# Kernel optimization log

Hardware: AMD Instinct MI355X
Metric: run time of the kernel (lower is better)

The kernel has to match this reference:

```python
import jax, jax.numpy as jnp
import numpy as np

N = 4096        # atoms
F = 128         # node feature channels (MACE hidden irreps scalar channels)
K = 8           # radial basis size
NELEM = 10      # chemical elements
RMAX = 5.0      # cutoff (Angstrom), model.r_max
BOX = 34.5      # box side -> ~0.1 atoms/A^3, ~50 neighbors within RMAX


def setup_inputs() -> dict:
    key = jax.random.key(0)
    ks = jax.random.split(key, 7)
    positions = jax.random.uniform(ks[0], (N, 3), jnp.float32) * BOX
    z = jax.random.randint(ks[1], (N,), 0, NELEM)
    embed = jax.random.normal(ks[2], (NELEM, F), jnp.float32) * 0.1
    W1 = jax.random.normal(ks[3], (K, F, F), jnp.float32) / np.sqrt(K * F)
    W2 = jax.random.normal(ks[4], (K, F, F), jnp.float32) / np.sqrt(K * F)
    Wr1 = jax.random.normal(ks[5], (F, F), jnp.float32) / np.sqrt(F)
    Wr2 = jax.random.normal(ks[6], (F, 1), jnp.float32) / np.sqrt(F)
    return dict(positions=positions, z=z, embed=embed, W1=W1, W2=W2, Wr1=Wr1, Wr2=Wr2)


def _energy(positions, embed, W1, W2, Wr1, Wr2, z):
    # node embedding from atomic species (node_attrs one-hot @ embedding)
    h = embed[z]                                            # [N,F]
    # --- neighborlist: radius graph with self-edge masking (pbc = False) ---
    sq = jnp.sum(positions * positions, axis=-1)            # [N]
    d2 = sq[:, None] + sq[None, :] - 2.0 * (positions @ positions.T)  # [N,N]
    eye = jnp.eye(positions.shape[0], dtype=bool)
    d2_safe = jnp.where(eye | (d2 <= 0), 1.0, d2)           # avoid sqrt(0) grad
    d = jnp.sqrt(d2_safe)                                   # [N,N]
    mask = (d < RMAX) & (~eye) & (d2 > 0)                   # keep_edge = ~true_self_edge
    # smooth cutoff envelope
    env = jnp.where(mask, 0.5 * (jnp.cos(jnp.pi * d / RMAX) + 1.0), 0.0)  # [N,N]
    # Gaussian radial basis
    mus = jnp.linspace(0.0, RMAX, K, dtype=jnp.float32)     # [K]
    gamma = jnp.float32((K / RMAX) ** 2)
    rbf = jnp.exp(-gamma * (d[..., None] - mus) ** 2) * env[..., None]    # [N,N,K]
    # --- two message-passing layers (radial-weighted neighbor aggregation) ---
    for W in (W1, W2):
        A = jnp.einsum('ijk,jf->ikf', rbf, h)               # [N,K,F] gather-scatter agg
        h = jax.nn.silu(jnp.einsum('ikf,kfg->ig', A, W) + h)  # [N,F]
    # --- per-atom energy readout, summed over graph ---
    e_atom = (jax.nn.silu(h @ Wr1) @ Wr2)[:, 0]             # [N]
    return jnp.sum(e_atom)


def reference(positions, z, embed, W1, W2, Wr1, Wr2):
    energy, dE_dpos = jax.value_and_grad(_energy)(positions, embed, W1, W2, Wr1, Wr2, z)
    forces = -dE_dpos                                       # [N,3]
    return energy, forces
```

## Files before the change

### kernel.cpp

```cpp
#include <hip/hip_runtime.h>
#include <math.h>

#define N_ATOMS 4096
#define F 128
#define K 8
#define KF 1024
#define KFF 131072
#define FF 16384
#define NF 524288
#define NKF 4194304
#define MAXNB 128
#define RMAX 5.0f
#define RMAX2 25.0f
#define GAMMA 2.56f
#define MU_STEP 0.714285714285714f
#define PI_F 3.14159265358979323846f
#define POR (PI_F / RMAX)

typedef __bf16 bf16x8_t __attribute__((ext_vector_type(8)));
typedef float f32x4_t __attribute__((ext_vector_type(4)));
typedef unsigned short u16x8_t __attribute__((ext_vector_type(8)));
typedef unsigned short u16x4_t __attribute__((ext_vector_type(4)));

__device__ __forceinline__ float sigm(float x){ return 1.0f/(1.0f + expf(-x)); }
__device__ __forceinline__ unsigned short f2bf(float x){
  unsigned int u = __float_as_uint(x);
  u += 0x7fff + ((u >> 16) & 1);
  return (unsigned short)(u >> 16);
}


__device__ __forceinline__ void agg_body(int a, int t,
        const float* __restrict__ h_in, const int* __restrict__ nb_idx,
        const float* __restrict__ rbf, const int* __restrict__ nb_cnt,
        unsigned short* __restrict__ Af){
  int grp = t >> 6, lane = t & 63;
  __shared__ int s_j[MAXNB];
  __shared__ float s_acc[4][8][128];
  int cnt = nb_cnt[a];
  for (int idx = t; idx < cnt; idx += 256) s_j[idx] = nb_idx[a*MAXNB + idx];
  __syncthreads();
  float2 acc[8];
  #pragma unroll
  for (int k = 0; k < 8; k++) acc[k] = {0.f, 0.f};
  const float4* rb = (const float4*)(rbf + (size_t)a*MAXNB*8);
  for (int n = grp; n < cnt; n += 4){
    float2 hv = *(const float2*)&h_in[(size_t)s_j[n]*F + lane*2];
    float4 r0 = rb[n*2], r1 = rb[n*2+1];
    acc[0].x += r0.x*hv.x; acc[0].y += r0.x*hv.y;
    acc[1].x += r0.y*hv.x; acc[1].y += r0.y*hv.y;
    acc[2].x += r0.z*hv.x; acc[2].y += r0.z*hv.y;
    acc[3].x += r0.w*hv.x; acc[3].y += r0.w*hv.y;
    acc[4].x += r1.x*hv.x; acc[4].y += r1.x*hv.y;
    acc[5].x += r1.y*hv.x; acc[5].y += r1.y*hv.y;
    acc[6].x += r1.z*hv.x; acc[6].y += r1.z*hv.y;
    acc[7].x += r1.w*hv.x; acc[7].y += r1.w*hv.y;
  }
  #pragma unroll
  for (int k = 0; k < 8; k++)
    *(float2*)&s_acc[grp][k][lane*2] = acc[k];
  __syncthreads();
  int k = t >> 5, q = t & 31;
  int f0 = q*4;
  float v[4];
  #pragma unroll
  for (int i = 0; i < 4; i++){
    int f = f0 + i;
    v[i] = s_acc[0][k][f] + s_acc[1][k][f] + s_acc[2][k][f] + s_acc[3][k][f];
  }
  int lf = (a & 15) | (((f0 >> 3) & 3) << 4);
  int kc = k*4 + (f0 >> 5);
  size_t flat = (size_t)(a >> 4)*16384 + ((size_t)kc*64 + lf)*8 + (f0 & 7);
  u16x4_t o;
  o[0] = f2bf(v[0]); o[1] = f2bf(v[1]); o[2] = f2bf(v[2]); o[3] = f2bf(v[3]);
  *(u16x4_t*)(Af + flat) = o;
}

__device__ __forceinline__ void mgemm_bwd_body(int bx, int t,
        const unsigned short* __restrict__ Gf, const unsigned short* __restrict__ Bf,
        unsigned short* __restrict__ dAbf){
  int l = t & 63, w = t >> 6;
  int rtile = (bx & 63)*4 + w;
  int nt0 = (bx >> 6)*8;
  f32x4_t acc[8];
  #pragma unroll
  for (int i = 0; i < 8; i++) acc[i] = (f32x4_t){0.f,0.f,0.f,0.f};
  const unsigned short* Ab = Gf + (size_t)rtile*2048 + l*8;
  const unsigned short* Bb = Bf + l*8;
  #pragma unroll
  for (int kc = 0; kc < 4; kc++){
    bf16x8_t a = *(const bf16x8_t*)(Ab + kc*512);
    #pragma unroll
    for (int nt = 0; nt < 8; nt++){
      bf16x8_t b = *(const bf16x8_t*)(Bb + (kc*64 + nt0 + nt)*512);
      acc[nt] = __builtin_amdgcn_mfma_f32_16x16x32_bf16(a, b, acc[nt], 0, 0, 0);
    }
  }
  int row0 = rtile*16 + (l >> 4)*4;
  int col = l & 15;
  #pragma unroll
  for (int nt = 0; nt < 8; nt++){
    #pragma unroll
    for (int r = 0; r < 4; r++)
      dAbf[(size_t)(row0+r)*1024 + (nt0+nt)*16 + col] = f2bf(acc[nt][r]);
  }
}


__global__ __launch_bounds__(256) void k_prep(const float* __restrict__ pos,
        const int* __restrict__ z, const float* __restrict__ embed,
        const float* __restrict__ W1, const float* __restrict__ W2,
        const float* __restrict__ Wr1,
        int* __restrict__ nb_idx, float* __restrict__ nb_d, int* __restrict__ nb_cnt,
        float* __restrict__ rbf, float* __restrict__ drbf,
        unsigned short* __restrict__ WF1, unsigned short* __restrict__ WF2,
        unsigned short* __restrict__ WDF2, unsigned short* __restrict__ WTF1,
        unsigned short* __restrict__ WTF2, unsigned short* __restrict__ Wr1F,
        unsigned short* __restrict__ Wr1TF,
        float* __restrict__ h0, unsigned short* __restrict__ h0bf){
  int t = threadIdx.x;
  if (blockIdx.x < 1024){
    int w = t >> 6, lane = t & 63;
    int i = blockIdx.x*4 + w;
    __shared__ float spx[256], spy[256], spz[256], ssq[256];
    float pix = pos[3*i], piy = pos[3*i+1], piz = pos[3*i+2];
    float sqi = pix*pix + piy*piy + piz*piz;
    int count = 0;
    for (int jb = 0; jb < N_ATOMS; jb += 256){
      __syncthreads();
      float px = pos[3*(jb+t)], py = pos[3*(jb+t)+1], pz = pos[3*(jb+t)+2];
      spx[t] = px; spy[t] = py; spz[t] = pz;
      ssq[t] = px*px + py*py + pz*pz;
      __syncthreads();
      #pragma unroll
      for (int c = 0; c < 4; c++){
        int jj = c*64 + lane;
        int j = jb + jj;
        float dot = pix*spx[jj] + piy*spy[jj] + piz*spz[jj];
        float d2 = sqi + ssq[jj] - 2.0f*dot;
        bool pred = (j != i) && (d2 > 0.0f) && (d2 < RMAX2);
        unsigned long long m = __ballot(pred);
        int off = __popcll(m & ((1ull << lane) - 1ull));
        if (pred){
          int p = count + off;
          if (p < MAXNB){ nb_idx[i*MAXNB + p] = j; nb_d[i*MAXNB + p] = sqrtf(d2); }
        }
        count += __popcll(m);
      }
    }
    int cc = count > MAXNB ? MAXNB : count;
    if (lane == 0) nb_cnt[i] = cc;
    __syncthreads();
    for (int n = lane; n < cc; n += 64){
      float d = nb_d[i*MAXNB + n];
      float ph = POR*d;
      float cph, sph;
      __sincosf(ph, &sph, &cph);
      float env = 0.5f*(cph + 1.0f);
      float denv = -0.5f*POR*sph;
      float rr[8], dd[8];
      #pragma unroll
      for (int k = 0; k < 8; k++){
        float dm = d - MU_STEP*(float)k;
        float G = expf(-GAMMA*dm*dm);
        rr[k] = G*env;
        dd[k] = G*(-2.0f*GAMMA*dm*env + denv);
      }
      float4* rb = (float4*)(rbf + ((size_t)i*MAXNB + n)*8);
      rb[0] = {rr[0],rr[1],rr[2],rr[3]};
      rb[1] = {rr[4],rr[5],rr[6],rr[7]};
      float4* db = (float4*)(drbf + ((size_t)i*MAXNB + n)*8);
      db[0] = {dd[0],dd[1],dd[2],dd[3]};
      db[1] = {dd[4],dd[5],dd[6],dd[7]};
    }
    return;
  }
  if (blockIdx.x >= 1088){
    int idx = (blockIdx.x - 1088)*256 + t;
    int i = idx >> 7, f = idx & 127;
    float v = embed[z[i]*F + f];
    h0[idx] = v;
    h0bf[idx] = f2bf(v);
    return;
  }
  int idx = (blockIdx.x - 1024)*256 + t;
  int l = idx & 63;
  int hi = idx >> 6;
  {
    int kc = hi >> 3, nt = hi & 7;
    int kfb = kc*32 + ((l>>4)&3)*8;
    int g = nt*16 + (l&15);
    u16x8_t v1, v2, vd;
    #pragma unroll
    for (int j = 0; j < 8; j++){
      int kf = kfb + j;
      v1[j] = f2bf(W1[kf*128 + g]);
      v2[j] = f2bf(W2[kf*128 + g]);
      vd[j] = f2bf(W2[(kf>>7)*FF + g*F + (kf&127)]);
    }
    *(u16x8_t*)(WF1 + idx*8) = v1;
    *(u16x8_t*)(WF2 + idx*8) = v2;
    *(u16x8_t*)(WDF2 + idx*8) = vd;
  }
  {
    int kc = hi >> 6, nt = hi & 63;
    int gb = kc*32 + ((l>>4)&3)*8;
    int kf = nt*16 + (l&15);
    u16x8_t t1, t2;
    #pragma unroll
    for (int j = 0; j < 8; j++){
      int g = gb + j;
      t1[j] = f2bf(W1[kf*128 + g]);
      t2[j] = f2bf(W2[kf*128 + g]);
    }
    *(u16x8_t*)(WTF1 + idx*8) = t1;
    *(u16x8_t*)(WTF2 + idx*8) = t2;
  }
  {
    int m = idx >> 9;
    int ll = (idx >> 3) & 63;
    int j = idx & 7;
    int kc = m >> 3, nt = m & 7;
    int kf = kc*32 + ((ll>>4)&3)*8 + j;
    int g = nt*16 + (ll&15);
    Wr1F[idx]  = f2bf(Wr1[kf*128 + g]);
    Wr1TF[idx] = f2bf(Wr1[g*128 + kf]);
  }
}

__global__ __launch_bounds__(256) void k_agg(const float* __restrict__ h_in,
        const int* __restrict__ nb_idx, const float* __restrict__ rbf,
        const int* __restrict__ nb_cnt, unsigned short* __restrict__ Af){
  agg_body(blockIdx.x, threadIdx.x, h_in, nb_idx, rbf, nb_cnt, Af);
}

__global__ __launch_bounds__(256) void k_bwdmix(const unsigned short* __restrict__ Gf,
        const unsigned short* __restrict__ Bf, unsigned short* __restrict__ dAbf,
        const float* __restrict__ g2b, const int* __restrict__ nb_idx,
        const float* __restrict__ rbf, const int* __restrict__ nb_cnt,
        unsigned short* __restrict__ Af){
  if (blockIdx.x < 512){
    mgemm_bwd_body(blockIdx.x, threadIdx.x, Gf, Bf, dAbf);
    return;
  }
  agg_body(blockIdx.x - 512, threadIdx.x, g2b, nb_idx, rbf, nb_cnt, Af);
}

__global__ __launch_bounds__(256) void k_mgemm_bwd(const unsigned short* __restrict__ Gf,
        const unsigned short* __restrict__ Bf, unsigned short* __restrict__ dAbf){
  mgemm_bwd_body(blockIdx.x, threadIdx.x, Gf, Bf, dAbf);
}

__global__ __launch_bounds__(256) void k_mgemm_fwd(const unsigned short* __restrict__ Af,
        const unsigned short* __restrict__ Bf, const float* __restrict__ addv,
        const float* __restrict__ msrc, float* __restrict__ out_m,
        float* __restrict__ out_h, unsigned short* __restrict__ out_hbf,
        unsigned short* __restrict__ out_frag, int mode){
  int t = threadIdx.x;
  int l = t & 63, w = t >> 6;
  int rtile = blockIdx.x;
  int nt = blockIdx.y*4 + w;
  f32x4_t accA = (f32x4_t){0.f,0.f,0.f,0.f};
  f32x4_t accB = (f32x4_t){0.f,0.f,0.f,0.f};
  const unsigned short* Ab = Af + (size_t)rtile*16384 + l*8;
  const unsigned short* Bb = Bf + l*8;
  #pragma unroll
  for (int kc = 0; kc < 32; kc += 2){
    bf16x8_t a0 = *(const bf16x8_t*)(Ab + kc*512);
    bf16x8_t b0 = *(const bf16x8_t*)(Bb + (kc*8 + nt)*512);
    bf16x8_t a1 = *(const bf16x8_t*)(Ab + (kc+1)*512);
    bf16x8_t b1 = *(const bf16x8_t*)(Bb + ((kc+1)*8 + nt)*512);
    accA = __builtin_amdgcn_mfma_f32_16x16x32_bf16(a0, b0, accA, 0, 0, 0);
    accB = __builtin_amdgcn_mfma_f32_16x16x32_bf16(a1, b1, accB, 0, 0, 0);
  }
  f32x4_t acc = accA + accB;
  int row0 = rtile*16 + (l >> 4)*4;
  int col = nt*16 + (l & 15);
  if (mode == 0){
    #pragma unroll
    for (int r = 0; r < 4; r++){
      int i = row0 + r;
      float m = acc[r] + addv[(size_t)i*F + col];
      out_m[(size_t)i*F + col] = m;
      float h = m*sigm(m);
      out_h[(size_t)i*F + col] = h;
      out_hbf[(size_t)i*F + col] = f2bf(h);
    }
  } else {
    int kc2 = col >> 5;
    int lfr0 = (((col >> 3) & 3) << 4);
    int jj = col & 7;
    #pragma unroll
    for (int r = 0; r < 4; r++){
      int i = row0 + r;
      float mm = msrc[(size_t)i*F + col];
      float sg = sigm(mm);
      float gv = (acc[r] + addv[(size_t)i*F + col])*(sg*(1.f + mm*(1.f - sg)));
      int lfr = (i & 15) | lfr0;
      size_t flat = (((size_t)(i>>4)*4 + kc2)*64 + lfr)*8 + jj;
      out_frag[flat] = f2bf(gv);
    }
  }
}

__global__ __launch_bounds__(64) void k_readout(const unsigned short* __restrict__ h2bf,
        const float* __restrict__ m2, const unsigned short* __restrict__ Wr1F,
        const unsigned short* __restrict__ Wr1TF, const float* __restrict__ Wr2,
        float* __restrict__ e_at, float* __restrict__ g2,
        unsigned short* __restrict__ g2frag){
  int a0 = blockIdx.x*16;
  int l = threadIdx.x;
  int rl = l & 15;
  __shared__ unsigned short sdu[16][136];
  f32x4_t acc[8];
  #pragma unroll
  for (int nt = 0; nt < 8; nt++) acc[nt] = (f32x4_t){0.f,0.f,0.f,0.f};
  #pragma unroll
  for (int kc = 0; kc < 4; kc++){
    bf16x8_t af = *(const bf16x8_t*)(h2bf + (size_t)(a0+rl)*F + kc*32 + ((l>>4)&3)*8);
    #pragma unroll
    for (int nt = 0; nt < 8; nt++){
      bf16x8_t bf = *(const bf16x8_t*)(Wr1F + ((kc*8+nt)*64 + l)*8);
      acc[nt] = __builtin_amdgcn_mfma_f32_16x16x32_bf16(af, bf, acc[nt], 0, 0, 0);
    }
  }
  float epart[4] = {0.f,0.f,0.f,0.f};
  #pragma unroll
  for (int nt = 0; nt < 8; nt++){
    float w2 = Wr2[nt*16 + rl];
    #pragma unroll
    for (int r = 0; r < 4; r++){
      float u = acc[nt][r];
      float sg = sigm(u);
      epart[r] += u*sg*w2;
      sdu[(l>>4)*4 + r][nt*16 + rl] = f2bf(w2*(sg*(1.f + u*(1.f - sg))));
    }
  }
  #pragma unroll
  for (int o = 1; o < 16; o <<= 1){
    #pragma unroll
    for (int r = 0; r < 4; r++) epart[r] += __shfl_xor(epart[r], o);
  }
  if (rl == 0){
    #pragma unroll
    for (int r = 0; r < 4; r++) e_at[a0 + (l>>4)*4 + r] = epart[r];
  }
  __syncthreads();
  f32x4_t acc2[8];
  #pragma unroll
  for (int nt = 0; nt < 8; nt++) acc2[nt] = (f32x4_t){0.f,0.f,0.f,0.f};
  #pragma unroll
  for (int kc = 0; kc < 4; kc++){
    bf16x8_t af = *(const bf16x8_t*)&sdu[rl][kc*32 + ((l>>4)&3)*8];
    #pragma unroll
    for (int nt = 0; nt < 8; nt++){
      bf16x8_t bf = *(const bf16x8_t*)(Wr1TF + ((kc*8+nt)*64 + l)*8);
      acc2[nt] = __builtin_amdgcn_mfma_f32_16x16x32_bf16(af, bf, acc2[nt], 0, 0, 0);
    }
  }
  #pragma unroll
  for (int nt = 0; nt < 8; nt++){
    int g = nt*16 + rl;
    int kc2 = g >> 5;
    int lfr0 = (((g >> 3) & 3) << 4);
    int jj = g & 7;
    #pragma unroll
    for (int r = 0; r < 4; r++){
      int a = a0 + (l>>4)*4 + r;
      float mm = m2[(size_t)a*F + g];
      float sg = sigm(mm);
      float gv = acc2[nt][r]*(sg*(1.f + mm*(1.f - sg)));
      g2[(size_t)a*F + g] = gv;
      int lfr = (a & 15) | lfr0;
      g2frag[(((size_t)(a>>4)*4 + kc2)*64 + lfr)*8 + jj] = f2bf(gv);
    }
  }
}

__global__ __launch_bounds__(256) void k_edge(const unsigned short* __restrict__ dA2bf,
        const unsigned short* __restrict__ dA1bf, const unsigned short* __restrict__ h1bf,
        const unsigned short* __restrict__ h0bf, const float* __restrict__ drbf,
        const int* __restrict__ nb_idx, const int* __restrict__ nb_cnt,
        float* __restrict__ edge_s){
  int a = blockIdx.x;
  int t = threadIdx.x;
  int w = t >> 6, l = t & 63;
  __shared__ int s_j[MAXNB];
  int cnt = nb_cnt[a];
  for (int idx = t; idx < cnt; idx += 256) s_j[idx] = nb_idx[a*MAXNB + idx];
  int r = l & 15;
  int sel = (l >> 4) & 3;
  u16x8_t a2u[4], a1u[4];
  #pragma unroll
  for (int kc = 0; kc < 4; kc++){
    u16x8_t v2 = {0,0,0,0,0,0,0,0};
    u16x8_t v1 = {0,0,0,0,0,0,0,0};
    if (r < 8){
      v2 = *(const u16x8_t*)(dA2bf + (size_t)a*KF + r*F + kc*32 + sel*8);
      v1 = *(const u16x8_t*)(dA1bf + (size_t)a*KF + r*F + kc*32 + sel*8);
    }
    a2u[kc] = v2; a1u[kc] = v1;
  }
  __syncthreads();
  for (int n0 = w*16; n0 < cnt; n0 += 64){
    int nl = n0 + r;
    int nls = nl < cnt ? nl : cnt - 1;
    int j = s_j[nls];
    const unsigned short* h1p = h1bf + (size_t)j*F + sel*8;
    const unsigned short* h0p = h0bf + (size_t)j*F + sel*8;
    f32x4_t acc = (f32x4_t){0.f,0.f,0.f,0.f};
    #pragma unroll
    for (int kc = 0; kc < 4; kc++){
      bf16x8_t b = *(const bf16x8_t*)(h1p + kc*32);
      acc = __builtin_amdgcn_mfma_f32_16x16x32_bf16(*(const bf16x8_t*)&a2u[kc], b, acc, 0, 0, 0);
    }
    #pragma unroll
    for (int kc = 0; kc < 4; kc++){
      bf16x8_t b = *(const bf16x8_t*)(h0p + kc*32);
      acc = __builtin_amdgcn_mfma_f32_16x16x32_bf16(*(const bf16x8_t*)&a1u[kc], b, acc, 0, 0, 0);
    }
    int krow = (l >> 4) * 4;
    float part = 0.f;
    if (krow < 8){
      float4 dr = *(const float4*)(drbf + ((size_t)a*MAXNB + nls)*8 + krow);
      part = acc[0]*dr.x + acc[1]*dr.y + acc[2]*dr.z + acc[3]*dr.w;
    }
    part += __shfl_xor(part, 16);
    if (l < 16 && nl < cnt) edge_s[a*MAXNB + nl] = part;
  }
}

__global__ __launch_bounds__(64) void k_force(const float* __restrict__ pos,
        const int* __restrict__ nb_idx, const float* __restrict__ nb_d,
        const int* __restrict__ nb_cnt, const float* __restrict__ edge_s,
        const float* __restrict__ e_at, float* __restrict__ out){
  int a = blockIdx.x;
  int lane = threadIdx.x;
  if (a == N_ATOMS){
    float s = 0.f;
    for (int i = lane; i < N_ATOMS; i += 64) s += e_at[i];
    #pragma unroll
    for (int o = 1; o < 64; o <<= 1) s += __shfl_xor(s, o);
    if (lane == 0) out[0] = s;
    return;
  }
  float pax = pos[3*a], pay = pos[3*a+1], paz = pos[3*a+2];
  int cnt = nb_cnt[a];
  float fx = 0.f, fy = 0.f, fz = 0.f;
  for (int n = lane; n < cnt; n += 64){
    int j = nb_idx[a*MAXNB + n];
    float d = nb_d[a*MAXNB + n];
    float s = edge_s[a*MAXNB + n];
    int cj = nb_cnt[j];
    int lo = 0, hi = cj - 1, p = -1;
    while (lo <= hi){
      int mid = (lo + hi) >> 1;
      int v = nb_idx[j*MAXNB + mid];
      if (v == a){ p = mid; break; }
      if (v < a) lo = mid + 1; else hi = mid - 1;
    }
    float sj = (p >= 0) ? edge_s[j*MAXNB + p] : 0.0f;
    float coef = (s + sj)/d;
    float dx = pax - pos[3*j], dy = pay - pos[3*j+1], dz = paz - pos[3*j+2];
    fx -= coef*dx; fy -= coef*dy; fz -= coef*dz;
  }
  #pragma unroll
  for (int o = 1; o < 64; o <<= 1){
    fx += __shfl_xor(fx, o); fy += __shfl_xor(fy, o); fz += __shfl_xor(fz, o);
  }
  if (lane == 0){
    out[1 + 3*a + 0] = fx;
    out[1 + 3*a + 1] = fy;
    out[1 + 3*a + 2] = fz;
  }
}

extern "C" void kernel_launch(void* const* d_in, const int* in_sizes, int n_in,
                              void* d_out, int out_size, void* d_ws, size_t ws_size,
                              hipStream_t stream){
  const float* pos   = (const float*)d_in[0];
  const int*   z     = (const int*)  d_in[1];
  const float* embed = (const float*)d_in[2];
  const float* W1    = (const float*)d_in[3];
  const float* W2    = (const float*)d_in[4];
  const float* Wr1   = (const float*)d_in[5];
  const float* Wr2   = (const float*)d_in[6];
  float* out = (float*)d_out;

  float* ws = (float*)d_ws;
  float* h0   = ws;
  float* h1   = h0 + NF;
  float* h2   = h1 + NF;
  float* m1   = h2 + NF;
  float* m2   = m1 + NF;
  float* g2b  = m2 + NF;
  float* Bbuf = g2b + NF;
  float* Cbuf = Bbuf + NKF;
  unsigned short* dA2bf = (unsigned short*)Bbuf;
  unsigned short* dA1bf = (unsigned short*)Cbuf;
  unsigned short* Afrag = (unsigned short*)(Cbuf + NKF);
  unsigned short* Gfrag = Afrag + NKF;
  unsigned short* h0bf = Gfrag + NF;
  unsigned short* h1bf = h0bf + NF;
  unsigned short* h2bf = h1bf + NF;
  unsigned short* WF1  = h2bf + NF;
  unsigned short* WF2  = WF1 + KFF;
  unsigned short* WDF2 = WF2 + KFF;
  unsigned short* WTF1 = WDF2 + KFF;
  unsigned short* WTF2 = WTF1 + KFF;
  unsigned short* Wr1F  = WTF2 + KFF;
  unsigned short* Wr1TF = Wr1F + FF;
  float* e_at = (float*)(Wr1TF + FF);
  float* nb_d = e_at + N_ATOMS;
  float* edge_s = nb_d + N_ATOMS*MAXNB;
  float* rbf  = edge_s + N_ATOMS*MAXNB;
  float* drbf = rbf + N_ATOMS*MAXNB*8;
  int* nb_idx = (int*)(drbf + N_ATOMS*MAXNB*8);
  int* nb_cnt = nb_idx + N_ATOMS*MAXNB;

  k_prep<<<1024 + 64 + NF/256, 256, 0, stream>>>(pos, z, embed, W1, W2, Wr1,
        nb_idx, nb_d, nb_cnt, rbf, drbf,
        WF1, WF2, WDF2, WTF1, WTF2, Wr1F, Wr1TF, h0, h0bf);

  k_agg<<<N_ATOMS, 256, 0, stream>>>(h0, nb_idx, rbf, nb_cnt, Afrag);
  k_mgemm_fwd<<<dim3(256, 2), 256, 0, stream>>>(Afrag, WF1, h0, h0, m1, h1, h1bf, Gfrag, 0);
  k_agg<<<N_ATOMS, 256, 0, stream>>>(h1, nb_idx, rbf, nb_cnt, Afrag);
  k_mgemm_fwd<<<dim3(256, 2), 256, 0, stream>>>(Afrag, WF2, h1, h1, m2, h2, h2bf, Gfrag, 0);

  k_readout<<<N_ATOMS/16, 64, 0, stream>>>(h2bf, m2, Wr1F, Wr1TF, Wr2, e_at, g2b, Gfrag);

  k_bwdmix<<<512 + N_ATOMS, 256, 0, stream>>>(Gfrag, WTF2, dA2bf,
        g2b, nb_idx, rbf, nb_cnt, Afrag);
  k_mgemm_fwd<<<dim3(256, 2), 256, 0, stream>>>(Afrag, WDF2, g2b, m1, m1, m1, h2bf, Gfrag, 1);
  k_mgemm_bwd<<<512, 256, 0, stream>>>(Gfrag, WTF1, dA1bf);
  k_edge<<<N_ATOMS, 256, 0, stream>>>(dA2bf, dA1bf, h1bf, h0bf, drbf, nb_idx, nb_cnt, edge_s);
  k_force<<<N_ATOMS + 1, 64, 0, stream>>>(pos, nb_idx, nb_d, nb_cnt, edge_s, e_at, out);
}
```

Baseline: 185.7 us.

## Gather bf16 features in aggregation, split neighbor search across two waves per atom

The neighbor aggregation kernels now gather bf16 copies of h0/h1 and of the readout gradient instead of fp32 rows. This halves the gather traffic, at the cost of precision on the aggregated features. The readout kernel additionally writes a row-major bf16 gradient buffer for this purpose. The neighbor-list build now has two waves scan the two halves of the atom range for each atom, staging candidates in shared memory before merging them. This doubles the parallelism of the O(N^2) search. The force kernel packs four atoms per 256-thread block to cut per-block launch overhead.

```diff
diff --git a/kernel.cpp b/kernel.cpp
--- a/kernel.cpp
+++ b/kernel.cpp
@@ -31,7 +31,7 @@
 
 
 __device__ __forceinline__ void agg_body(int a, int t,
-        const float* __restrict__ h_in, const int* __restrict__ nb_idx,
+        const unsigned short* __restrict__ h_in, const int* __restrict__ nb_idx,
         const float* __restrict__ rbf, const int* __restrict__ nb_cnt,
         unsigned short* __restrict__ Af){
   int grp = t >> 6, lane = t & 63;
@@ -45,16 +45,18 @@
   for (int k = 0; k < 8; k++) acc[k] = {0.f, 0.f};
   const float4* rb = (const float4*)(rbf + (size_t)a*MAXNB*8);
   for (int n = grp; n < cnt; n += 4){
-    float2 hv = *(const float2*)&h_in[(size_t)s_j[n]*F + lane*2];
+    unsigned int pv = *(const unsigned int*)&h_in[(size_t)s_j[n]*F + lane*2];
+    float hx = __uint_as_float(pv << 16);
+    float hy = __uint_as_float(pv & 0xffff0000u);
     float4 r0 = rb[n*2], r1 = rb[n*2+1];
-    acc[0].x += r0.x*hv.x; acc[0].y += r0.x*hv.y;
-    acc[1].x += r0.y*hv.x; acc[1].y += r0.y*hv.y;
-    acc[2].x += r0.z*hv.x; acc[2].y += r0.z*hv.y;
-    acc[3].x += r0.w*hv.x; acc[3].y += r0.w*hv.y;
-    acc[4].x += r1.x*hv.x; acc[4].y += r1.x*hv.y;
-    acc[5].x += r1.y*hv.x; acc[5].y += r1.y*hv.y;
-    acc[6].x += r1.z*hv.x; acc[6].y += r1.z*hv.y;
-    acc[7].x += r1.w*hv.x; acc[7].y += r1.w*hv.y;
+    acc[0].x += r0.x*hx; acc[0].y += r0.x*hy;
+    acc[1].x += r0.y*hx; acc[1].y += r0.y*hy;
+    acc[2].x += r0.z*hx; acc[2].y += r0.z*hy;
+    acc[3].x += r0.w*hx; acc[3].y += r0.w*hy;
+    acc[4].x += r1.x*hx; acc[4].y += r1.x*hy;
+    acc[5].x += r1.y*hx; acc[5].y += r1.y*hy;
+    acc[6].x += r1.z*hx; acc[6].y += r1.z*hy;
+    acc[7].x += r1.w*hx; acc[7].y += r1.w*hy;
   }
   #pragma unroll
   for (int k = 0; k < 8; k++)
@@ -119,40 +121,60 @@
         unsigned short* __restrict__ Wr1TF,
         float* __restrict__ h0, unsigned short* __restrict__ h0bf){
   int t = threadIdx.x;
-  if (blockIdx.x < 1024){
-    int w = t >> 6, lane = t & 63;
-    int i = blockIdx.x*4 + w;
-    __shared__ float spx[256], spy[256], spz[256], ssq[256];
+  if (blockIdx.x < 2048){
+    int w2 = t >> 7;
+    int half = (t >> 6) & 1;
+    int lane = t & 63;
+    int i = blockIdx.x*2 + w2;
+    __shared__ float spx[2][256], spy[2][256], spz[2][256], ssq[2][256];
+    __shared__ int s_jl[2][2][128];
+    __shared__ float s_dl[2][2][128];
+    __shared__ int s_cnt[2][2];
     float pix = pos[3*i], piy = pos[3*i+1], piz = pos[3*i+2];
     float sqi = pix*pix + piy*piy + piz*piz;
     int count = 0;
-    for (int jb = 0; jb < N_ATOMS; jb += 256){
+    for (int it = 0; it < 8; it++){
       __syncthreads();
-      float px = pos[3*(jb+t)], py = pos[3*(jb+t)+1], pz = pos[3*(jb+t)+2];
-      spx[t] = px; spy[t] = py; spz[t] = pz;
-      ssq[t] = px*px + py*py + pz*pz;
+      {
+        int j0 = it*256 + t;
+        float px = pos[3*j0], py = pos[3*j0+1], pz = pos[3*j0+2];
+        spx[0][t] = px; spy[0][t] = py; spz[0][t] = pz;
+        ssq[0][t] = px*px + py*py + pz*pz;
+        int j1 = 2048 + it*256 + t;
+        px = pos[3*j1]; py = pos[3*j1+1]; pz = pos[3*j1+2];
+        spx[1][t] = px; spy[1][t] = py; spz[1][t] = pz;
+        ssq[1][t] = px*px + py*py + pz*pz;
+      }
       __syncthreads();
       #pragma unroll
       for (int c = 0; c < 4; c++){
         int jj = c*64 + lane;
-        int j = jb + jj;
-        float dot = pix*spx[jj] + piy*spy[jj] + piz*spz[jj];
-        float d2 = sqi + ssq[jj] - 2.0f*dot;
+        int j = half*2048 + it*256 + jj;
+        float dot = pix*spx[half][jj] + piy*spy[half][jj] + piz*spz[half][jj];
+        float d2 = sqi + ssq[half][jj] - 2.0f*dot;
         bool pred = (j != i) && (d2 > 0.0f) && (d2 < RMAX2);
         unsigned long long m = __ballot(pred);
         int off = __popcll(m & ((1ull << lane) - 1ull));
         if (pred){
           int p = count + off;
-          if (p < MAXNB){ nb_idx[i*MAXNB + p] = j; nb_d[i*MAXNB + p] = sqrtf(d2); }
+          if (p < 128){ s_jl[w2][half][p] = j; s_dl[w2][half][p] = sqrtf(d2); }
         }
         count += __popcll(m);
       }
     }
-    int cc = count > MAXNB ? MAXNB : count;
-    if (lane == 0) nb_cnt[i] = cc;
+    if (lane == 0) s_cnt[w2][half] = count;
     __syncthreads();
-    for (int n = lane; n < cc; n += 64){
-      float d = nb_d[i*MAXNB + n];
+    int c0 = s_cnt[w2][0]; if (c0 > 128) c0 = 128;
+    int c1 = s_cnt[w2][1]; if (c1 > 128) c1 = 128;
+    int cc = c0 + c1; if (cc > MAXNB) cc = MAXNB;
+    int tia = t & 127;
+    if (tia == 0) nb_cnt[i] = cc;
+    for (int n = tia; n < cc; n += 128){
+      int j; float d;
+      if (n < c0){ j = s_jl[w2][0][n]; d = s_dl[w2][0][n]; }
+      else       { j = s_jl[w2][1][n - c0]; d = s_dl[w2][1][n - c0]; }
+      nb_idx[i*MAXNB + n] = j;
+      nb_d[i*MAXNB + n] = d;
       float ph = POR*d;
       float cph, sph;
       __sincosf(ph, &sph, &cph);
@@ -175,15 +197,15 @@
     }
     return;
   }
-  if (blockIdx.x >= 1088){
-    int idx = (blockIdx.x - 1088)*256 + t;
+  if (blockIdx.x >= 2112){
+    int idx = (blockIdx.x - 2112)*256 + t;
     int i = idx >> 7, f = idx & 127;
     float v = embed[z[i]*F + f];
     h0[idx] = v;
     h0bf[idx] = f2bf(v);
     return;
   }
-  int idx = (blockIdx.x - 1024)*256 + t;
+  int idx = (blockIdx.x - 2048)*256 + t;
   int l = idx & 63;
   int hi = idx >> 6;
   {
@@ -228,7 +250,7 @@
   }
 }
 
-__global__ __launch_bounds__(256) void k_agg(const float* __restrict__ h_in,
+__global__ __launch_bounds__(256) void k_agg(const unsigned short* __restrict__ h_in,
         const int* __restrict__ nb_idx, const float* __restrict__ rbf,
         const int* __restrict__ nb_cnt, unsigned short* __restrict__ Af){
   agg_body(blockIdx.x, threadIdx.x, h_in, nb_idx, rbf, nb_cnt, Af);
@@ -236,14 +258,14 @@
 
 __global__ __launch_bounds__(256) void k_bwdmix(const unsigned short* __restrict__ Gf,
         const unsigned short* __restrict__ Bf, unsigned short* __restrict__ dAbf,
-        const float* __restrict__ g2b, const int* __restrict__ nb_idx,
+        const unsigned short* __restrict__ g2bf, const int* __restrict__ nb_idx,
         const float* __restrict__ rbf, const int* __restrict__ nb_cnt,
         unsigned short* __restrict__ Af){
   if (blockIdx.x < 512){
     mgemm_bwd_body(blockIdx.x, threadIdx.x, Gf, Bf, dAbf);
     return;
   }
-  agg_body(blockIdx.x - 512, threadIdx.x, g2b, nb_idx, rbf, nb_cnt, Af);
+  agg_body(blockIdx.x - 512, threadIdx.x, g2bf, nb_idx, rbf, nb_cnt, Af);
 }
 
 __global__ __launch_bounds__(256) void k_mgemm_bwd(const unsigned short* __restrict__ Gf,
@@ -307,7 +329,7 @@
         const float* __restrict__ m2, const unsigned short* __restrict__ Wr1F,
         const unsigned short* __restrict__ Wr1TF, const float* __restrict__ Wr2,
         float* __restrict__ e_at, float* __restrict__ g2,
-        unsigned short* __restrict__ g2frag){
+        unsigned short* __restrict__ g2bf, unsigned short* __restrict__ g2frag){
   int a0 = blockIdx.x*16;
   int l = threadIdx.x;
   int rl = l & 15;
@@ -371,8 +393,10 @@
       float sg = sigm(mm);
       float gv = acc2[nt][r]*(sg*(1.f + mm*(1.f - sg)));
       g2[(size_t)a*F + g] = gv;
+      unsigned short gb = f2bf(gv);
+      g2bf[(size_t)a*F + g] = gb;
       int lfr = (a & 15) | lfr0;
-      g2frag[(((size_t)(a>>4)*4 + kc2)*64 + lfr)*8 + jj] = f2bf(gv);
+      g2frag[(((size_t)(a>>4)*4 + kc2)*64 + lfr)*8 + jj] = gb;
     }
   }
 }
@@ -430,20 +454,22 @@
   }
 }
 
-__global__ __launch_bounds__(64) void k_force(const float* __restrict__ pos,
+__global__ __launch_bounds__(256) void k_force(const float* __restrict__ pos,
         const int* __restrict__ nb_idx, const float* __restrict__ nb_d,
         const int* __restrict__ nb_cnt, const float* __restrict__ edge_s,
         const float* __restrict__ e_at, float* __restrict__ out){
-  int a = blockIdx.x;
-  int lane = threadIdx.x;
-  if (a == N_ATOMS){
-    float s = 0.f;
-    for (int i = lane; i < N_ATOMS; i += 64) s += e_at[i];
-    #pragma unroll
-    for (int o = 1; o < 64; o <<= 1) s += __shfl_xor(s, o);
-    if (lane == 0) out[0] = s;
+  int bw = threadIdx.x >> 6, lane = threadIdx.x & 63;
+  if (blockIdx.x == N_ATOMS/4){
+    if (bw == 0){
+      float s = 0.f;
+      for (int i = lane; i < N_ATOMS; i += 64) s += e_at[i];
+      #pragma unroll
+      for (int o = 1; o < 64; o <<= 1) s += __shfl_xor(s, o);
+      if (lane == 0) out[0] = s;
+    }
     return;
   }
+  int a = blockIdx.x*4 + bw;
   float pax = pos[3*a], pay = pos[3*a+1], paz = pos[3*a+2];
   int cnt = nb_cnt[a];
   float fx = 0.f, fy = 0.f, fz = 0.f;
@@ -503,7 +529,8 @@
   unsigned short* h0bf = Gfrag + NF;
   unsigned short* h1bf = h0bf + NF;
   unsigned short* h2bf = h1bf + NF;
-  unsigned short* WF1  = h2bf + NF;
+  unsigned short* g2bf = h2bf + NF;
+  unsigned short* WF1  = g2bf + NF;
   unsigned short* WF2  = WF1 + KFF;
   unsigned short* WDF2 = WF2 + KFF;
   unsigned short* WTF1 = WDF2 + KFF;
@@ -518,21 +545,21 @@
   int* nb_idx = (int*)(drbf + N_ATOMS*MAXNB*8);
   int* nb_cnt = nb_idx + N_ATOMS*MAXNB;
 
-  k_prep<<<1024 + 64 + NF/256, 256, 0, stream>>>(pos, z, embed, W1, W2, Wr1,
+  k_prep<<<2048 + 64 + NF/256, 256, 0, stream>>>(pos, z, embed, W1, W2, Wr1,
         nb_idx, nb_d, nb_cnt, rbf, drbf,
         WF1, WF2, WDF2, WTF1, WTF2, Wr1F, Wr1TF, h0, h0bf);
 
-  k_agg<<<N_ATOMS, 256, 0, stream>>>(h0, nb_idx, rbf, nb_cnt, Afrag);
+  k_agg<<<N_ATOMS, 256, 0, stream>>>(h0bf, nb_idx, rbf, nb_cnt, Afrag);
   k_mgemm_fwd<<<dim3(256, 2), 256, 0, stream>>>(Afrag, WF1, h0, h0, m1, h1, h1bf, Gfrag, 0);
-  k_agg<<<N_ATOMS, 256, 0, stream>>>(h1, nb_idx, rbf, nb_cnt, Afrag);
+  k_agg<<<N_ATOMS, 256, 0, stream>>>(h1bf, nb_idx, rbf, nb_cnt, Afrag);
   k_mgemm_fwd<<<dim3(256, 2), 256, 0, stream>>>(Afrag, WF2, h1, h1, m2, h2, h2bf, Gfrag, 0);
 
-  k_readout<<<N_ATOMS/16, 64, 0, stream>>>(h2bf, m2, Wr1F, Wr1TF, Wr2, e_at, g2b, Gfrag);
+  k_readout<<<N_ATOMS/16, 64, 0, stream>>>(h2bf, m2, Wr1F, Wr1TF, Wr2, e_at, g2b, g2bf, Gfrag);
 
   k_bwdmix<<<512 + N_ATOMS, 256, 0, stream>>>(Gfrag, WTF2, dA2bf,
-        g2b, nb_idx, rbf, nb_cnt, Afrag);
+        g2bf, nb_idx, rbf, nb_cnt, Afrag);
   k_mgemm_fwd<<<dim3(256, 2), 256, 0, stream>>>(Afrag, WDF2, g2b, m1, m1, m1, h2bf, Gfrag, 1);
   k_mgemm_bwd<<<512, 256, 0, stream>>>(Gfrag, WTF1, dA1bf);
   k_edge<<<N_ATOMS, 256, 0, stream>>>(dA2bf, dA1bf, h1bf, h0bf, drbf, nb_idx, nb_cnt, edge_s);
-  k_force<<<N_ATOMS + 1, 64, 0, stream>>>(pos, nb_idx, nb_d, nb_cnt, edge_s, e_at, out);
-}
+  k_force<<<N_ATOMS/4 + 1, 256, 0, stream>>>(pos, nb_idx, nb_d, nb_cnt, edge_s, e_at, out);
+}
```

After: 187.3 us, median of 2. Within noise of the previous version (+0.9%).
